# Performance work log

Measured on AMD Instinct MI355X. Metric: run time of the kernel, lower is better.

Reference implementation:

```python
import jax, jax.numpy as jnp
import numpy as np

EMBED_DIM = 768
FFN_DIM = 3072
N_WIRES = 10


def setup_inputs() -> dict:
    key = jax.random.key(0)
    ks = jax.random.split(key, 7)
    x = jax.random.normal(ks[0], (8, 2048, EMBED_DIM), dtype=jnp.float32)
    # map_to_wires: nn.Linear(embed_dim, n_wires, bias=False) -> weight [n_wires, embed_dim]
    W_map = jax.random.normal(ks[1], (N_WIRES, EMBED_DIM), dtype=jnp.float32) / np.sqrt(EMBED_DIM)
    # trainable RY rotation angles, one per wire
    theta = jax.random.uniform(ks[2], (N_WIRES,), dtype=jnp.float32, minval=-np.pi, maxval=np.pi)
    W1 = jax.random.normal(ks[3], (FFN_DIM, N_WIRES), dtype=jnp.float32) / np.sqrt(N_WIRES)
    b1 = jnp.zeros((FFN_DIM,), dtype=jnp.float32)
    W2 = jax.random.normal(ks[4], (EMBED_DIM, FFN_DIM), dtype=jnp.float32) / np.sqrt(FFN_DIM)
    b2 = jnp.zeros((EMBED_DIM,), dtype=jnp.float32)
    return {"x": x, "W_map": W_map, "theta": theta, "W1": W1, "b1": b1, "W2": W2, "b2": b2}


def reference(x, W_map, theta, W1, b1, W2, b2):
    batch, seq_len, embed_dim = x.shape
    x_flat = x.reshape(batch * seq_len, embed_dim)            # [F, E]
    x_wires = x_flat @ W_map.T                                 # [F, W]
    # Quantum circuit: per wire i, state RY(theta_i) RX(x_i) |0>.
    # All gates are single-qubit on the |0...0> product state, so the
    # register stays a product state and <Z_i> reduces exactly to
    # cos(theta_i) * cos(x_i) (same math as the full 2^n statevector sim).
    q_out = jnp.cos(theta)[None, :] * jnp.cos(x_wires)         # [F, W]
    h = jax.nn.relu(q_out @ W1.T + b1)                         # [F, FFN]
    out = h @ W2.T + b2                                        # [F, E]
    return out.reshape(batch, seq_len, embed_dim)
```

## Files before the change

### kernel.cpp

```cpp
#include <hip/hip_runtime.h>


typedef __attribute__((ext_vector_type(4))) float f32x4;
typedef __attribute__((ext_vector_type(8))) short bf16x8;

#define F_TOTAL 16384
#define E_DIM   768
#define FFN     3072

static __device__ __forceinline__ unsigned short f2bf(float f) {
    union { float f; unsigned int i; } v; v.f = f;
    unsigned int r = v.i + 0x7FFFu + ((v.i >> 16) & 1u);
    return (unsigned short)(r >> 16);
}
static __device__ __forceinline__ void gload16(const void* g, void* l) {
    __builtin_amdgcn_global_load_lds((const __attribute__((address_space(1))) unsigned int*)g,
                                     (__attribute__((address_space(3))) unsigned int*)l,
                                     16, 0, 0);
}

__global__ __launch_bounds__(384) void kW2(const float* __restrict__ w2,
                                           unsigned short* __restrict__ w2b) {
    const int n = (int)blockIdx.x;
    const int c = (int)threadIdx.x;
    const float4* src = (const float4*)(w2 + (size_t)n * FFN + c * 8);
    float4 a = src[0], b = src[1];
    bf16x8 v;
    v[0] = (short)f2bf(a.x); v[1] = (short)f2bf(a.y);
    v[2] = (short)f2bf(a.z); v[3] = (short)f2bf(a.w);
    v[4] = (short)f2bf(b.x); v[5] = (short)f2bf(b.y);
    v[6] = (short)f2bf(b.z); v[7] = (short)f2bf(b.w);
    *(bf16x8*)(w2b + (size_t)n * FFN + (size_t)(c ^ (n & 7)) * 8) = v;
}

__global__ void kP(const float* __restrict__ w1,
                   const float* __restrict__ b1,
                   unsigned short* __restrict__ w1p) {
    int k = blockIdx.x * 256 + threadIdx.x;
    if (k >= FFN) return;
    float r[32];
#pragma unroll
    for (int w = 0; w < 10; ++w) r[w] = w1[k * 10 + w];
    r[10] = b1[k];
#pragma unroll
    for (int w = 11; w < 32; ++w) r[w] = 0.f;
#pragma unroll
    for (int c = 0; c < 4; ++c) {
        bf16x8 v;
#pragma unroll
        for (int e = 0; e < 8; ++e) v[e] = (short)f2bf(r[c * 8 + e]);
        *(bf16x8*)(w1p + (size_t)k * 32 + (size_t)((c ^ (k & 3)) * 8)) = v;
    }
}

__global__ __launch_bounds__(256) void kQ(const float* __restrict__ x,
                                          const float* __restrict__ wm,
                                          const float* __restrict__ th,
                                          unsigned short* __restrict__ qp) {
    __shared__ float wms[10 * 768];
    const int tid = (int)threadIdx.x;
    for (int i = tid; i < 10 * 768; i += 256) wms[i] = wm[i];
    __syncthreads();

    const int wv = tid >> 6, l = tid & 63;
    const int mbase = (int)blockIdx.x * 16 + wv * 4;
    const float thv = (l < 10) ? th[l] : 0.f;
    const float cth = __cosf(thv);

#pragma unroll
    for (int r = 0; r < 4; ++r) {
        const int m = mbase + r;
        const float4* xp = (const float4*)(x + (size_t)m * E_DIM);
        const float4 xa = xp[l], xb = xp[64 + l], xc = xp[128 + l];
        float s[10];
#pragma unroll
        for (int w = 0; w < 10; ++w) {
            const float4* wp = (const float4*)(wms + w * E_DIM);
            const float4 wa = wp[l], wb = wp[64 + l], wc = wp[128 + l];
            float t0 = xa.x * wa.x;
            float t1 = xa.y * wa.y;
            t0 = fmaf(xa.z, wa.z, t0); t1 = fmaf(xa.w, wa.w, t1);
            t0 = fmaf(xb.x, wb.x, t0); t1 = fmaf(xb.y, wb.y, t1);
            t0 = fmaf(xb.z, wb.z, t0); t1 = fmaf(xb.w, wb.w, t1);
            t0 = fmaf(xc.x, wc.x, t0); t1 = fmaf(xc.y, wc.y, t1);
            t0 = fmaf(xc.z, wc.z, t0); t1 = fmaf(xc.w, wc.w, t1);
            s[w] = t0 + t1;
        }
#pragma unroll
        for (int w = 0; w < 10; ++w) {
            float v = s[w];
            v += __shfl_xor(v, 1);  v += __shfl_xor(v, 2);  v += __shfl_xor(v, 4);
            v += __shfl_xor(v, 8);  v += __shfl_xor(v, 16); v += __shfl_xor(v, 32);
            s[w] = v;
        }
        if (l < 32) {
            float sv = 0.f;
#pragma unroll
            for (int w = 0; w < 10; ++w) sv = (l == w) ? s[w] : sv;
            float val = (l < 10) ? (cth * __cosf(sv)) : ((l == 10) ? 1.0f : 0.f);
            qp[(size_t)m * 32 + (size_t)((((l >> 3) ^ (m & 3)) * 8) + (l & 7))] = f2bf(val);
        }
    }
}

__global__ __launch_bounds__(512, 4) void kG(const unsigned short* __restrict__ w2b,
                                             const float* __restrict__ b2,
                                             const unsigned short* __restrict__ qp,
                                             const unsigned short* __restrict__ w1p,
                                             float* __restrict__ outp) {
    __shared__ __align__(16) unsigned short w2s[384 * 64];
    __shared__ __align__(16) unsigned short hs[64 * 64];
    __shared__ __align__(16) unsigned short qs[64 * 32];
    __shared__ __align__(16) unsigned short w1s[64 * 32];

    const int tid = (int)threadIdx.x;
    const int wv = tid >> 6;
    const int l  = tid & 63;
    const int bid = (int)blockIdx.x;
    const int ld  = (bid & 7) * 64 + (bid >> 3);
    const int m0 = (ld & 255) * 64;
    const int n0 = (ld >> 8) * 384;

    if (wv < 4) {
        const unsigned short* src = qp + (size_t)(m0 + (tid >> 2)) * 32 + (size_t)(tid & 3) * 8;
        gload16(src, qs + (size_t)wv * 512);
    }

    const f32x4 z4 = {0.f, 0.f, 0.f, 0.f};
    f32x4 acc[4][3];
#pragma unroll
    for (int a = 0; a < 4; ++a)
#pragma unroll
        for (int b = 0; b < 3; ++b) acc[a][b] = z4;

    const int mih = wv >> 1;
    const int r_w2 = tid >> 3;
    const int c_w2 = tid & 7;
    bf16x8 aq;

    for (int kt = 0; kt < FFN / 64; ++kt) {
        const int k0 = kt * 64;
        if (wv < 4) {
            const unsigned short* s1 = w1p + (size_t)(k0 + (tid >> 2)) * 32 + (size_t)(tid & 3) * 8;
            gload16(s1, w1s + (size_t)wv * 512);
        }
#pragma unroll
        for (int i = 0; i < 6; ++i) {
            int r = i * 64 + r_w2;
            const unsigned short* s2 = w2b + (size_t)(n0 + r) * FFN + k0 + (size_t)c_w2 * 8;
            gload16(s2, w2s + (size_t)i * 4096 + (size_t)wv * 512);
        }
        __syncthreads();

        if (kt == 0) {
            int qrow = mih * 16 + (l & 15);
            int qch = (l >> 4) ^ (qrow & 3);
            aq = *(const bf16x8*)(qs + qrow * 32 + qch * 8);
        }

#pragma unroll
        for (int j = 0; j < 2; ++j) {
            int ki = (wv * 2 + j) & 3;
            int kw = ki * 16 + (l & 15);
            int cw = (l >> 4) ^ (kw & 3);
            bf16x8 bw = *(const bf16x8*)(w1s + kw * 32 + cw * 8);
            f32x4 hv = __builtin_amdgcn_mfma_f32_16x16x32_bf16(aq, bw, z4, 0, 0, 0);
            int kkc = ki * 16 + (l & 15);
            int mb = mih * 16 + (l >> 4) * 4;
#pragma unroll
            for (int jj = 0; jj < 4; ++jj) {
                int m = mb + jj;
                hs[m * 64 + (((kkc >> 3) ^ (m & 7)) * 8) + (kkc & 7)] =
                    f2bf(fmaxf(hv[jj], 0.f));
            }
        }
        __syncthreads();

#pragma unroll
        for (int kk2 = 0; kk2 < 2; ++kk2) {
            const int kc = kk2 * 4 + (l >> 4);
            bf16x8 af[4];
#pragma unroll
            for (int mi = 0; mi < 4; ++mi) {
                int m = mi * 16 + (l & 15);
                af[mi] = *(const bf16x8*)(hs + m * 64 + ((kc ^ (m & 7)) * 8));
            }
#pragma unroll
            for (int ni = 0; ni < 3; ++ni) {
                int n = wv * 48 + ni * 16 + (l & 15);
                bf16x8 bfr = *(const bf16x8*)(w2s + n * 64 + ((kc ^ (n & 7)) * 8));
#pragma unroll
                for (int mi = 0; mi < 4; ++mi)
                    acc[mi][ni] = __builtin_amdgcn_mfma_f32_16x16x32_bf16(af[mi], bfr, acc[mi][ni], 0, 0, 0);
            }
        }
        __syncthreads();
    }

#pragma unroll
    for (int ni = 0; ni < 3; ++ni) {
        int n = n0 + wv * 48 + ni * 16 + (l & 15);
        float b2v = b2[n];
#pragma unroll
        for (int mi = 0; mi < 4; ++mi) {
            int mbase = m0 + mi * 16 + (l >> 4) * 4;
#pragma unroll
            for (int jj = 0; jj < 4; ++jj)
                outp[(size_t)(mbase + jj) * E_DIM + n] = acc[mi][ni][jj] + b2v;
        }
    }
}

extern "C" void kernel_launch(void* const* d_in, const int* in_sizes, int n_in,
                              void* d_out, int out_size, void* d_ws, size_t ws_size,
                              hipStream_t stream) {
    const float* x    = (const float*)d_in[0];
    const float* wmap = (const float*)d_in[1];
    const float* th   = (const float*)d_in[2];
    const float* w1   = (const float*)d_in[3];
    const float* b1   = (const float*)d_in[4];
    const float* w2   = (const float*)d_in[5];
    const float* b2   = (const float*)d_in[6];
    float* out = (float*)d_out;

    unsigned short* qp  = (unsigned short*)d_ws;
    unsigned short* w1p = qp + (size_t)F_TOTAL * 32;
    unsigned short* w2b = w1p + (size_t)FFN * 32;

    kW2<<<E_DIM, 384, 0, stream>>>(w2, w2b);
    kP<<<(FFN + 255) / 256, 256, 0, stream>>>(w1, b1, w1p);
    kQ<<<1024, 256, 0, stream>>>(x, wmap, th, qp);
    kG<<<512, 512, 0, stream>>>(w2b, b2, qp, w1p, out);
}
```

Baseline: 124.0 us.

## Double-buffer W2 tiles, enlarge M tile to 128, load W1/q fragments into registers

The fused GEMM kernel now processes 128 rows per block instead of 64, halving the grid and doubling the reuse of each W2 tile staged in LDS. W2 tiles are double-buffered so the next K-step's global->LDS loads overlap the current step's MFMAs. Each wave fetches its W1 and q fragments straight into registers with inline asm instead of through shared memory, and priority is raised around the MFMA block. It costs more registers and LDS (occupancy bound drops to 2 blocks per CU), and 256 blocks may underfill the CUs.

```diff
diff --git a/kernel.cpp b/kernel.cpp
--- a/kernel.cpp
+++ b/kernel.cpp
@@ -103,110 +103,125 @@
     }
 }
 
-__global__ __launch_bounds__(512, 4) void kG(const unsigned short* __restrict__ w2b,
+__global__ __launch_bounds__(512, 2) void kG(const unsigned short* __restrict__ w2b,
                                              const float* __restrict__ b2,
                                              const unsigned short* __restrict__ qp,
                                              const unsigned short* __restrict__ w1p,
                                              float* __restrict__ outp) {
-    __shared__ __align__(16) unsigned short w2s[384 * 64];
-    __shared__ __align__(16) unsigned short hs[64 * 64];
-    __shared__ __align__(16) unsigned short qs[64 * 32];
-    __shared__ __align__(16) unsigned short w1s[64 * 32];
+    __shared__ __align__(16) unsigned short w2s[2][384 * 64];
+    __shared__ __align__(16) unsigned short hs[128 * 64];
 
     const int tid = (int)threadIdx.x;
-    const int wv = tid >> 6;
-    const int l  = tid & 63;
+    const int wv = tid >> 6, l = tid & 63;
     const int bid = (int)blockIdx.x;
-    const int ld  = (bid & 7) * 64 + (bid >> 3);
-    const int m0 = (ld & 255) * 64;
-    const int n0 = (ld >> 8) * 384;
-
-    if (wv < 4) {
-        const unsigned short* src = qp + (size_t)(m0 + (tid >> 2)) * 32 + (size_t)(tid & 3) * 8;
-        gload16(src, qs + (size_t)wv * 512);
-    }
+    const int x8 = bid & 7, yb = bid >> 3;
+    const int m0 = ((x8 & 3) * 32 + yb) * 128;
+    const int n0 = (x8 >> 2) * 384;
+
+    const int rw = tid >> 3, cw = tid & 7;
+    const int wr = wv >> 2, wc = wv & 3;
+
+#define STAGE(BUF, KT) do { int k0_ = (KT) * 64;                                   \
+    _Pragma("unroll") for (int i_ = 0; i_ < 6; ++i_) {                             \
+        int r_ = i_ * 64 + rw;                                                     \
+        gload16(w2b + (size_t)(n0 + r_) * FFN + k0_ + (size_t)cw * 8,              \
+                (unsigned short*)w2s[BUF] + i_ * 4096 + wv * 512); } } while (0)
+
+#define LOADW1(D, KT, KI) do {                                                     \
+    const unsigned short* a_ = w1p + (size_t)((KT) * 64 + (KI) * 16 + (l & 15)) * 32 \
+                                   + (size_t)(((l >> 4) ^ (l & 3)) * 8);           \
+    asm volatile("global_load_dwordx4 %0, %1, off" : "=v"(D) : "v"(a_)); } while (0)
+
+    bf16x8 aq;
+    {
+        const unsigned short* qa = qp + (size_t)(m0 + wv * 16 + (l & 15)) * 32
+                                      + (size_t)(((l >> 4) ^ (l & 3)) * 8);
+        asm volatile("global_load_dwordx4 %0, %1, off" : "=v"(aq) : "v"(qa));
+    }
+    bf16x8 f0, f1, f2, f3, g0, g1, g2, g3;
+    STAGE(0, 0);
+    LOADW1(f0, 0, 0); LOADW1(f1, 0, 1); LOADW1(f2, 0, 2); LOADW1(f3, 0, 3);
 
     const f32x4 z4 = {0.f, 0.f, 0.f, 0.f};
-    f32x4 acc[4][3];
+    f32x4 acc[4][6];
 #pragma unroll
     for (int a = 0; a < 4; ++a)
 #pragma unroll
-        for (int b = 0; b < 3; ++b) acc[a][b] = z4;
-
-    const int mih = wv >> 1;
-    const int r_w2 = tid >> 3;
-    const int c_w2 = tid & 7;
-    bf16x8 aq;
-
-    for (int kt = 0; kt < FFN / 64; ++kt) {
-        const int k0 = kt * 64;
-        if (wv < 4) {
-            const unsigned short* s1 = w1p + (size_t)(k0 + (tid >> 2)) * 32 + (size_t)(tid & 3) * 8;
-            gload16(s1, w1s + (size_t)wv * 512);
-        }
-#pragma unroll
-        for (int i = 0; i < 6; ++i) {
-            int r = i * 64 + r_w2;
-            const unsigned short* s2 = w2b + (size_t)(n0 + r) * FFN + k0 + (size_t)c_w2 * 8;
-            gload16(s2, w2s + (size_t)i * 4096 + (size_t)wv * 512);
-        }
-        __syncthreads();
-
-        if (kt == 0) {
-            int qrow = mih * 16 + (l & 15);
-            int qch = (l >> 4) ^ (qrow & 3);
-            aq = *(const bf16x8*)(qs + qrow * 32 + qch * 8);
-        }
-
-#pragma unroll
-        for (int j = 0; j < 2; ++j) {
-            int ki = (wv * 2 + j) & 3;
-            int kw = ki * 16 + (l & 15);
-            int cw = (l >> 4) ^ (kw & 3);
-            bf16x8 bw = *(const bf16x8*)(w1s + kw * 32 + cw * 8);
-            f32x4 hv = __builtin_amdgcn_mfma_f32_16x16x32_bf16(aq, bw, z4, 0, 0, 0);
-            int kkc = ki * 16 + (l & 15);
-            int mb = mih * 16 + (l >> 4) * 4;
-#pragma unroll
-            for (int jj = 0; jj < 4; ++jj) {
-                int m = mb + jj;
-                hs[m * 64 + (((kkc >> 3) ^ (m & 7)) * 8) + (kkc & 7)] =
-                    f2bf(fmaxf(hv[jj], 0.f));
+        for (int b = 0; b < 6; ++b) acc[a][b] = z4;
+
+    int cur = 0;
+    for (int t = 0; t < 48; ++t) {
+        asm volatile("s_waitcnt vmcnt(0)" ::: "memory");
+        __builtin_amdgcn_sched_barrier(0);
+        __builtin_amdgcn_s_barrier();
+        __builtin_amdgcn_sched_barrier(0);
+
+        if (t < 47) {
+            STAGE(cur ^ 1, t + 1);
+            LOADW1(g0, t + 1, 0); LOADW1(g1, t + 1, 1);
+            LOADW1(g2, t + 1, 2); LOADW1(g3, t + 1, 3);
+        }
+
+        f32x4 hv0 = __builtin_amdgcn_mfma_f32_16x16x32_bf16(aq, f0, z4, 0, 0, 0);
+        f32x4 hv1 = __builtin_amdgcn_mfma_f32_16x16x32_bf16(aq, f1, z4, 0, 0, 0);
+        f32x4 hv2 = __builtin_amdgcn_mfma_f32_16x16x32_bf16(aq, f2, z4, 0, 0, 0);
+        f32x4 hv3 = __builtin_amdgcn_mfma_f32_16x16x32_bf16(aq, f3, z4, 0, 0, 0);
+        {
+            const int hrow = wv * 16 + (l >> 4) * 4;
+#define HWR(HV, KI) do { int c_ = (KI) * 16 + (l & 15); int cp_ = c_ >> 3;         \
+    _Pragma("unroll") for (int jj_ = 0; jj_ < 4; ++jj_) { int m_ = hrow + jj_;     \
+        hs[m_ * 64 + ((cp_ ^ (m_ & 7)) * 8) + (c_ & 7)] = f2bf(fmaxf(HV[jj_], 0.f)); } } while (0)
+            HWR(hv0, 0); HWR(hv1, 1); HWR(hv2, 2); HWR(hv3, 3);
+#undef HWR
+        }
+
+        asm volatile("s_waitcnt lgkmcnt(0)" ::: "memory");
+        __builtin_amdgcn_sched_barrier(0);
+        __builtin_amdgcn_s_barrier();
+        __builtin_amdgcn_sched_barrier(0);
+
+        {
+            const unsigned short* w2c = (const unsigned short*)w2s[cur];
+#pragma unroll
+            for (int kk2 = 0; kk2 < 2; ++kk2) {
+                const int kc = kk2 * 4 + (l >> 4);
+                bf16x8 af[4], bfr[6];
+#pragma unroll
+                for (int mi = 0; mi < 4; ++mi) {
+                    int m_ = wr * 64 + mi * 16 + (l & 15);
+                    af[mi] = *(const bf16x8*)(hs + m_ * 64 + ((kc ^ (m_ & 7)) * 8));
+                }
+#pragma unroll
+                for (int ni = 0; ni < 6; ++ni) {
+                    int n_ = wc * 96 + ni * 16 + (l & 15);
+                    bfr[ni] = *(const bf16x8*)(w2c + n_ * 64 + ((kc ^ (n_ & 7)) * 8));
+                }
+                __builtin_amdgcn_s_setprio(1);
+#pragma unroll
+                for (int ni = 0; ni < 6; ++ni)
+#pragma unroll
+                    for (int mi = 0; mi < 4; ++mi)
+                        acc[mi][ni] = __builtin_amdgcn_mfma_f32_16x16x32_bf16(af[mi], bfr[ni], acc[mi][ni], 0, 0, 0);
+                __builtin_amdgcn_s_setprio(0);
             }
         }
-        __syncthreads();
-
-#pragma unroll
-        for (int kk2 = 0; kk2 < 2; ++kk2) {
-            const int kc = kk2 * 4 + (l >> 4);
-            bf16x8 af[4];
-#pragma unroll
-            for (int mi = 0; mi < 4; ++mi) {
-                int m = mi * 16 + (l & 15);
-                af[mi] = *(const bf16x8*)(hs + m * 64 + ((kc ^ (m & 7)) * 8));
-            }
-#pragma unroll
-            for (int ni = 0; ni < 3; ++ni) {
-                int n = wv * 48 + ni * 16 + (l & 15);
-                bf16x8 bfr = *(const bf16x8*)(w2s + n * 64 + ((kc ^ (n & 7)) * 8));
-#pragma unroll
-                for (int mi = 0; mi < 4; ++mi)
-                    acc[mi][ni] = __builtin_amdgcn_mfma_f32_16x16x32_bf16(af[mi], bfr, acc[mi][ni], 0, 0, 0);
-            }
-        }
-        __syncthreads();
-    }
-
-#pragma unroll
-    for (int ni = 0; ni < 3; ++ni) {
-        int n = n0 + wv * 48 + ni * 16 + (l & 15);
+
+        f0 = g0; f1 = g1; f2 = g2; f3 = g3;
+        cur ^= 1;
+    }
+#undef STAGE
+#undef LOADW1
+
+#pragma unroll
+    for (int ni = 0; ni < 6; ++ni) {
+        int n = n0 + wc * 96 + ni * 16 + (l & 15);
         float b2v = b2[n];
 #pragma unroll
         for (int mi = 0; mi < 4; ++mi) {
-            int mbase = m0 + mi * 16 + (l >> 4) * 4;
+            int mb = m0 + wr * 64 + mi * 16 + (l >> 4) * 4;
 #pragma unroll
             for (int jj = 0; jj < 4; ++jj)
-                outp[(size_t)(mbase + jj) * E_DIM + n] = acc[mi][ni][jj] + b2v;
+                outp[(size_t)(mb + jj) * E_DIM + n] = acc[mi][ni][jj] + b2v;
         }
     }
 }
@@ -230,5 +245,5 @@
     kW2<<<E_DIM, 384, 0, stream>>>(w2, w2b);
     kP<<<(FFN + 255) / 256, 256, 0, stream>>>(w1, b1, w1p);
     kQ<<<1024, 256, 0, stream>>>(x, wmap, th, qp);
-    kG<<<512, 512, 0, stream>>>(w2b, b2, qp, w1p, out);
-}
+    kG<<<256, 512, 0, stream>>>(w2b, b2, qp, w1p, out);
+}
```

After: 127.5 us. +2.8%, slower.
